# Kernel optimization log

Measured on AMD Instinct MI355X. Metric: run time of the kernel, lower is better.

The kernel has to match this reference:

```python
import jax, jax.numpy as jnp
import numpy as np

N_NODES, N_EDGES, N_GRAPHS = 20000, 640000, 16
D_NODE = D_EDGE = D_GLOBAL = 64
IN_DIM, LATENT, OUT_DIM = 256, 128, 64


def setup_inputs() -> dict:
    key = jax.random.key(0)
    ks = jax.random.split(key, 12)
    node_attr = jax.random.normal(ks[0], (N_NODES, D_NODE), dtype=jnp.float32)
    edge_attr = jax.random.normal(ks[1], (N_EDGES, D_EDGE), dtype=jnp.float32)
    global_attr = jax.random.normal(ks[2], (N_GRAPHS, D_GLOBAL), dtype=jnp.float32)
    node_mask = jax.random.uniform(ks[3], (N_NODES,), dtype=jnp.float32)
    edge_mask = jax.random.uniform(ks[4], (N_EDGES,), dtype=jnp.float32)
    edge_index = jax.random.randint(ks[5], (2, N_EDGES), 0, N_NODES, dtype=jnp.int64)
    eg_index = jax.random.randint(ks[6], (N_EDGES,), 0, N_GRAPHS, dtype=jnp.int64)
    # MLP params: Linear(IN_DIM, LATENT) -> ReLU -> Linear(LATENT, OUT_DIM)
    s1 = 1.0 / np.sqrt(IN_DIM)
    s2 = 1.0 / np.sqrt(LATENT)
    W1 = jax.random.uniform(ks[7], (IN_DIM, LATENT), minval=-s1, maxval=s1, dtype=jnp.float32)
    b1 = jax.random.uniform(ks[8], (LATENT,), minval=-s1, maxval=s1, dtype=jnp.float32)
    W2 = jax.random.uniform(ks[9], (LATENT, OUT_DIM), minval=-s2, maxval=s2, dtype=jnp.float32)
    b2 = jax.random.uniform(ks[10], (OUT_DIM,), minval=-s2, maxval=s2, dtype=jnp.float32)
    return {"node_attr": node_attr, "edge_attr": edge_attr, "global_attr": global_attr,
            "node_mask": node_mask, "edge_mask": edge_mask,
            "edge_index": edge_index, "eg_index": eg_index,
            "W1": W1, "b1": b1, "W2": W2, "b2": b2}


def reference(node_attr, edge_attr, global_attr, node_mask, edge_mask,
              edge_index, eg_index, W1, b1, W2, b2):
    senders, receivers = edge_index[0], edge_index[1]
    masked_nodes = node_attr * node_mask[:, None]          # [N, d_n]
    senders_attr = masked_nodes[senders]                   # [E, d_n] gather
    receivers_attr = masked_nodes[receivers]               # [E, d_n] gather
    globals_exp = global_attr[eg_index]                    # [E, d_g] gather
    collected = jnp.concatenate(
        [edge_attr, senders_attr, receivers_attr, globals_exp], axis=-1)  # [E, IN_DIM]
    h = jax.nn.relu(collected @ W1 + b1)                   # [E, LATENT]
    out = h @ W2 + b2                                      # [E, OUT_DIM]
    return edge_mask[:, None] * out
```

## Files before the change

### kernel.cpp

```cpp
#include <hip/hip_runtime.h>
#include <stdint.h>

typedef __attribute__((ext_vector_type(8))) short short8;
typedef __attribute__((ext_vector_type(4))) float floatx4;
typedef unsigned short ushort_t;

#define E_TOTAL 640000
#define N_NODES 20000
#define M_BLK   128
#define N_TILES (E_TOTAL / M_BLK)
#define XS_LD   264
#define HS_LD   136

__device__ __forceinline__ unsigned short f2h(float f){
    _Float16 h = (_Float16)f;
    union { _Float16 h; unsigned short u; } v; v.h = h; return v.u;
}
__device__ __forceinline__ unsigned pk2h(float a, float b){
    return (unsigned)f2h(a) | ((unsigned)f2h(b) << 16);
}

__global__ void repack_w(const float* __restrict__ W1,
                         const float* __restrict__ W2,
                         ushort_t* __restrict__ W1p,
                         ushort_t* __restrict__ W2p){
    int tid = blockIdx.x * 256 + threadIdx.x;
    if (tid < 8*8*64){
        int kt = tid >> 9, nt = (tid >> 6) & 7, l = tid & 63;
        int q = l >> 4, c = l & 15;
        ushort_t tmp[8];
        #pragma unroll
        for (int j = 0; j < 8; j++)
            tmp[j] = f2h(W1[(kt*32 + q*8 + j)*128 + nt*16 + c]);
        #pragma unroll
        for (int j = 0; j < 8; j++) W1p[tid*8 + j] = tmp[j];
    } else if (tid < 8*8*64 + 4*4*64){
        int t = tid - 8*8*64;
        int kt = t >> 8, nt = (t >> 6) & 3, l = t & 63;
        int q = l >> 4, c = l & 15;
        ushort_t tmp[8];
        #pragma unroll
        for (int j = 0; j < 8; j++)
            tmp[j] = f2h(W2[(kt*32 + q*8 + j)*64 + nt*16 + c]);
        #pragma unroll
        for (int j = 0; j < 8; j++) W2p[t*8 + j] = tmp[j];
    }
}

__global__ void prep_tables(const float* __restrict__ node_attr,
                            const float* __restrict__ node_mask,
                            const float* __restrict__ global_attr,
                            ushort_t* __restrict__ node16,
                            ushort_t* __restrict__ glob16){
    int gid = blockIdx.x * 256 + threadIdx.x;
    if (gid < N_NODES * 8){
        int r = gid >> 3, c8 = gid & 7;
        float m = node_mask[r];
        const float4* src = (const float4*)(node_attr + (size_t)r*64 + c8*8);
        float4 a = src[0], b = src[1];
        uint4 o;
        o.x = pk2h(a.x*m, a.y*m); o.y = pk2h(a.z*m, a.w*m);
        o.z = pk2h(b.x*m, b.y*m); o.w = pk2h(b.z*m, b.w*m);
        *(uint4*)(node16 + (size_t)r*64 + c8*8) = o;
    } else if (gid < N_NODES * 8 + 16 * 8){
        int t = gid - N_NODES * 8;
        int r = t >> 3, c8 = t & 7;
        const float4* src = (const float4*)(global_attr + (size_t)r*64 + c8*8);
        float4 a = src[0], b = src[1];
        uint4 o;
        o.x = pk2h(a.x, a.y); o.y = pk2h(a.z, a.w);
        o.z = pk2h(b.x, b.y); o.w = pk2h(b.z, b.w);
        *(uint4*)(glob16 + (size_t)r*64 + c8*8) = o;
    }
}

__global__ __launch_bounds__(512, 4)
void edge_mlp(const float* __restrict__ edge_attr,
              const float* __restrict__ edge_mask,
              const int*   __restrict__ edge_index,
              const int*   __restrict__ eg_index,
              const float* __restrict__ b1,
              const float* __restrict__ b2,
              const ushort_t* __restrict__ W1p,
              const ushort_t* __restrict__ W2p,
              const ushort_t* __restrict__ node16,
              const ushort_t* __restrict__ glob16,
              float*       __restrict__ out){
    __shared__ ushort_t Xs[M_BLK * XS_LD];
    ushort_t* Hs = Xs;

    const int tid = threadIdx.x;
    const int e0  = blockIdx.x * M_BLK;
    const int w   = tid >> 6, lane = tid & 63;
    const int q   = lane >> 4, cc = lane & 15;
    const int mt0 = (w >> 2) * 4;
    const int nt0 = (w & 3) * 2;

    const short8* W1v = (const short8*)W1p;
    short8 wb[8][2];
    #pragma unroll
    for (int kt = 0; kt < 8; kt++)
        #pragma unroll
        for (int j = 0; j < 2; j++)
            wb[kt][j] = W1v[(kt*8 + nt0 + j)*64 + lane];

    {
        const float4* src = (const float4*)(edge_attr + (size_t)e0 * 64);
        #pragma unroll
        for (int k = 0; k < 4; k++){
            int idx = tid + k*512;
            int r = idx >> 4, c = idx & 15;
            float4 v = src[idx];
            uint2 o; o.x = pk2h(v.x, v.y); o.y = pk2h(v.z, v.w);
            *(uint2*)&Xs[r*XS_LD + c*4] = o;
        }
    }
    {
        #pragma unroll
        for (int k = 0; k < 2; k++){
            int idx = tid + k*512;
            int r = idx >> 3, c = idx & 7;
            int g = eg_index[e0 + r];
            uint4 v = *(const uint4*)(glob16 + (size_t)g*64 + c*8);
            *(uint4*)&Xs[r*XS_LD + 192 + c*8] = v;
        }
    }
    {
        int r = tid >> 2, seg = (tid >> 1) & 1, half = tid & 1;
        int idx = edge_index[seg*E_TOTAL + e0 + r];
        const uint4* nsrc = (const uint4*)(node16 + (size_t)idx*64 + half*32);
        ushort_t* dst = &Xs[r*XS_LD + 64 + seg*64 + half*32];
        #pragma unroll
        for (int c2 = 0; c2 < 4; c2++)
            *(uint4*)(dst + c2*8) = nsrc[c2];
    }
    __syncthreads();

    floatx4 acc[4][2];
    #pragma unroll
    for (int i = 0; i < 4; i++)
        #pragma unroll
        for (int j = 0; j < 2; j++) acc[i][j] = (floatx4){0.f,0.f,0.f,0.f};

    #pragma unroll
    for (int kt = 0; kt < 8; kt++){
        #pragma unroll
        for (int i = 0; i < 4; i++){
            const short8 a = *(const short8*)&Xs[((mt0 + i)*16 + cc)*XS_LD + kt*32 + q*8];
            #pragma unroll
            for (int j = 0; j < 2; j++)
                acc[i][j] = __builtin_amdgcn_mfma_f32_16x16x32_f16(a, wb[kt][j], acc[i][j], 0, 0, 0);
        }
    }
    __syncthreads();

    #pragma unroll
    for (int j = 0; j < 2; j++){
        int col = (nt0 + j)*16 + cc;
        float bb = b1[col];
        #pragma unroll
        for (int i = 0; i < 4; i++){
            int rowb = (mt0 + i)*16 + q*4;
            #pragma unroll
            for (int r = 0; r < 4; r++){
                float v = acc[i][j][r] + bb;
                v = v > 0.f ? v : 0.f;
                Hs[(rowb + r)*HS_LD + col] = f2h(v);
            }
        }
    }
    __syncthreads();

    const int mt20 = (w >> 1) * 2;
    const int nt20 = (w & 1) * 2;

    floatx4 acc2[2][2];
    #pragma unroll
    for (int i = 0; i < 2; i++)
        #pragma unroll
        for (int j = 0; j < 2; j++) acc2[i][j] = (floatx4){0.f,0.f,0.f,0.f};

    const short8* W2v = (const short8*)W2p;
    #pragma unroll
    for (int kt = 0; kt < 4; kt++){
        short8 b[2];
        #pragma unroll
        for (int j = 0; j < 2; j++) b[j] = W2v[(kt*4 + nt20 + j)*64 + lane];
        #pragma unroll
        for (int i = 0; i < 2; i++){
            const short8 a = *(const short8*)&Hs[((mt20 + i)*16 + cc)*HS_LD + kt*32 + q*8];
            #pragma unroll
            for (int j = 0; j < 2; j++)
                acc2[i][j] = __builtin_amdgcn_mfma_f32_16x16x32_f16(a, b[j], acc2[i][j], 0, 0, 0);
        }
    }

    float bb2[2];
    #pragma unroll
    for (int j = 0; j < 2; j++) bb2[j] = b2[(nt20 + j)*16 + cc];
    #pragma unroll
    for (int i = 0; i < 2; i++){
        #pragma unroll
        for (int r = 0; r < 4; r++){
            int row = (mt20 + i)*16 + q*4 + r;
            float em = edge_mask[e0 + row];
            size_t base = (size_t)(e0 + row) * 64;
            #pragma unroll
            for (int j = 0; j < 2; j++)
                out[base + (nt20 + j)*16 + cc] = (acc2[i][j][r] + bb2[j]) * em;
        }
    }
}

__global__ __launch_bounds__(512, 4)
void edge_mlp_fb(const float* __restrict__ node_attr,
                 const float* __restrict__ edge_attr,
                 const float* __restrict__ global_attr,
                 const float* __restrict__ node_mask,
                 const float* __restrict__ edge_mask,
                 const int*   __restrict__ edge_index,
                 const int*   __restrict__ eg_index,
                 const float* __restrict__ b1,
                 const float* __restrict__ b2,
                 const ushort_t* __restrict__ W1p,
                 const ushort_t* __restrict__ W2p,
                 float*       __restrict__ out){
    __shared__ ushort_t Xs[M_BLK * XS_LD];
    ushort_t* Hs = Xs;
    const int tid = threadIdx.x;
    const int e0  = blockIdx.x * M_BLK;
    {
        const float4* src = (const float4*)(edge_attr + (size_t)e0 * 64);
        #pragma unroll
        for (int k = 0; k < 4; k++){
            int idx = tid + k*512;
            int r = idx >> 4, c = idx & 15;
            float4 v = src[idx];
            uint2 o; o.x = pk2h(v.x, v.y); o.y = pk2h(v.z, v.w);
            *(uint2*)&Xs[r*XS_LD + c*4] = o;
        }
    }
    {
        #pragma unroll
        for (int k = 0; k < 4; k++){
            int idx = tid + k*512; int r = idx >> 4, c = idx & 15;
            int g = eg_index[e0 + r];
            const float4* src = (const float4*)(global_attr + (size_t)g * 64);
            float4 v = src[c];
            uint2 o; o.x = pk2h(v.x, v.y); o.y = pk2h(v.z, v.w);
            *(uint2*)&Xs[r*XS_LD + 192 + c*4] = o;
        }
    }
    {
        int r = tid >> 2, seg = (tid >> 1) & 1, half = tid & 1;
        int idx = edge_index[seg*E_TOTAL + e0 + r];
        float m = node_mask[idx];
        const float4* src = (const float4*)(node_attr + (size_t)idx * 64) + half*8;
        ushort_t* dst = &Xs[r*XS_LD + 64 + seg*64 + half*32];
        #pragma unroll
        for (int c2 = 0; c2 < 8; c2++){
            float4 v = src[c2];
            uint2 o; o.x = pk2h(v.x*m, v.y*m); o.y = pk2h(v.z*m, v.w*m);
            *(uint2*)(dst + c2*4) = o;
        }
    }
    __syncthreads();

    const int w  = tid >> 6, lane = tid & 63;
    const int q  = lane >> 4, cc = lane & 15;
    const int mt0 = (w >> 2) * 4;
    const int nt0 = (w & 3) * 2;

    floatx4 acc[4][2];
    #pragma unroll
    for (int i = 0; i < 4; i++)
        #pragma unroll
        for (int j = 0; j < 2; j++) acc[i][j] = (floatx4){0.f,0.f,0.f,0.f};

    const short8* W1v = (const short8*)W1p;
    #pragma unroll
    for (int kt = 0; kt < 8; kt++){
        short8 b[2];
        #pragma unroll
        for (int j = 0; j < 2; j++) b[j] = W1v[(kt*8 + nt0 + j)*64 + lane];
        #pragma unroll
        for (int i = 0; i < 4; i++){
            const short8 a = *(const short8*)&Xs[((mt0 + i)*16 + cc)*XS_LD + kt*32 + q*8];
            #pragma unroll
            for (int j = 0; j < 2; j++)
                acc[i][j] = __builtin_amdgcn_mfma_f32_16x16x32_f16(a, b[j], acc[i][j], 0, 0, 0);
        }
    }
    __syncthreads();

    #pragma unroll
    for (int j = 0; j < 2; j++){
        int col = (nt0 + j)*16 + cc;
        float bb = b1[col];
        #pragma unroll
        for (int i = 0; i < 4; i++){
            int rowb = (mt0 + i)*16 + q*4;
            #pragma unroll
            for (int r = 0; r < 4; r++){
                float v = acc[i][j][r] + bb;
                v = v > 0.f ? v : 0.f;
                Hs[(rowb + r)*HS_LD + col] = f2h(v);
            }
        }
    }
    __syncthreads();

    const int mt20 = (w >> 1) * 2;
    const int nt20 = (w & 1) * 2;

    floatx4 acc2[2][2];
    #pragma unroll
    for (int i = 0; i < 2; i++)
        #pragma unroll
        for (int j = 0; j < 2; j++) acc2[i][j] = (floatx4){0.f,0.f,0.f,0.f};

    const short8* W2v = (const short8*)W2p;
    #pragma unroll
    for (int kt = 0; kt < 4; kt++){
        short8 b[2];
        #pragma unroll
        for (int j = 0; j < 2; j++) b[j] = W2v[(kt*4 + nt20 + j)*64 + lane];
        #pragma unroll
        for (int i = 0; i < 2; i++){
            const short8 a = *(const short8*)&Hs[((mt20 + i)*16 + cc)*HS_LD + kt*32 + q*8];
            #pragma unroll
            for (int j = 0; j < 2; j++)
                acc2[i][j] = __builtin_amdgcn_mfma_f32_16x16x32_f16(a, b[j], acc2[i][j], 0, 0, 0);
        }
    }

    float bb2[2];
    #pragma unroll
    for (int j = 0; j < 2; j++) bb2[j] = b2[(nt20 + j)*16 + cc];
    #pragma unroll
    for (int i = 0; i < 2; i++){
        #pragma unroll
        for (int r = 0; r < 4; r++){
            int row = (mt20 + i)*16 + q*4 + r;
            float em = edge_mask[e0 + row];
            size_t base = (size_t)(e0 + row) * 64;
            #pragma unroll
            for (int j = 0; j < 2; j++)
                out[base + (nt20 + j)*16 + cc] = (acc2[i][j][r] + bb2[j]) * em;
        }
    }
}

extern "C" void kernel_launch(void* const* d_in, const int* in_sizes, int n_in,
                              void* d_out, int out_size, void* d_ws, size_t ws_size,
                              hipStream_t stream){
    const float* node_attr   = (const float*)d_in[0];
    const float* edge_attr   = (const float*)d_in[1];
    const float* global_attr = (const float*)d_in[2];
    const float* node_mask   = (const float*)d_in[3];
    const float* edge_mask   = (const float*)d_in[4];
    const int*   edge_index  = (const int*)d_in[5];
    const int*   eg_index    = (const int*)d_in[6];
    const float* W1          = (const float*)d_in[7];
    const float* b1          = (const float*)d_in[8];
    const float* W2          = (const float*)d_in[9];
    const float* b2          = (const float*)d_in[10];

    ushort_t* W1p = (ushort_t*)d_ws;
    ushort_t* W2p = W1p + 8*8*64*8;
    ushort_t* node16 = W2p + 4*4*64*8;
    ushort_t* glob16 = node16 + (size_t)N_NODES*64;

    size_t need = (size_t)(8*8*64*8 + 4*4*64*8 + N_NODES*64 + 16*64) * sizeof(ushort_t);

    repack_w<<<20, 256, 0, stream>>>(W1, W2, W1p, W2p);
    if (ws_size >= need){
        prep_tables<<<(N_NODES*8 + 16*8 + 255)/256, 256, 0, stream>>>(
            node_attr, node_mask, global_attr, node16, glob16);
        edge_mlp<<<N_TILES, 512, 0, stream>>>(
            edge_attr, edge_mask, edge_index, eg_index,
            b1, b2, W1p, W2p, node16, glob16, (float*)d_out);
    } else {
        edge_mlp_fb<<<N_TILES, 512, 0, stream>>>(
            node_attr, edge_attr, global_attr, node_mask, edge_mask,
            edge_index, eg_index, b1, b2, W1p, W2p, (float*)d_out);
    }
}
```

Before: 337.0 us.

## Split first GEMM K loop into two halves to halve LDS and raise occupancy

The 256-wide input tile is now staged in shared memory in two 128-column halves: edge_attr plus sender features first, then receiver plus global features. This cuts LDS per block from 128x264 to 128x136 halves. W1 fragments are loaded per k-step instead of being held for all 8 k-steps, which reduces register pressure. Together these allow launch_bounds to go from 4 to 8 blocks per CU. In exchange it adds two extra barriers, serializes the second gather after the first half of the MFMA work, and reloads weights from global/L2 inside the loop.

```diff
diff --git a/kernel.cpp b/kernel.cpp
--- a/kernel.cpp
+++ b/kernel.cpp
@@ -9,8 +9,9 @@
 #define N_NODES 20000
 #define M_BLK   128
 #define N_TILES (E_TOTAL / M_BLK)
+#define XS2_LD  132
+#define HS_LD   136
 #define XS_LD   264
-#define HS_LD   136
 
 __device__ __forceinline__ unsigned short f2h(float f){
     _Float16 h = (_Float16)f;
@@ -74,7 +75,7 @@
     }
 }
 
-__global__ __launch_bounds__(512, 4)
+__global__ __launch_bounds__(512, 8)
 void edge_mlp(const float* __restrict__ edge_attr,
               const float* __restrict__ edge_mask,
               const int*   __restrict__ edge_index,
@@ -86,8 +87,9 @@
               const ushort_t* __restrict__ node16,
               const ushort_t* __restrict__ glob16,
               float*       __restrict__ out){
-    __shared__ ushort_t Xs[M_BLK * XS_LD];
-    ushort_t* Hs = Xs;
+    __shared__ ushort_t S[M_BLK * HS_LD];
+    ushort_t* Xs = S;
+    ushort_t* Hs = S;
 
     const int tid = threadIdx.x;
     const int e0  = blockIdx.x * M_BLK;
@@ -97,12 +99,6 @@
     const int nt0 = (w & 3) * 2;
 
     const short8* W1v = (const short8*)W1p;
-    short8 wb[8][2];
-    #pragma unroll
-    for (int kt = 0; kt < 8; kt++)
-        #pragma unroll
-        for (int j = 0; j < 2; j++)
-            wb[kt][j] = W1v[(kt*8 + nt0 + j)*64 + lane];
 
     {
         const float4* src = (const float4*)(edge_attr + (size_t)e0 * 64);
@@ -112,44 +108,71 @@
             int r = idx >> 4, c = idx & 15;
             float4 v = src[idx];
             uint2 o; o.x = pk2h(v.x, v.y); o.y = pk2h(v.z, v.w);
-            *(uint2*)&Xs[r*XS_LD + c*4] = o;
-        }
-    }
+            *(uint2*)&Xs[r*XS2_LD + c*4] = o;
+        }
+        #pragma unroll
+        for (int k = 0; k < 2; k++){
+            int idx = tid + k*512;
+            int r = idx >> 3, c = idx & 7;
+            int ei = edge_index[e0 + r];
+            uint4 v = *(const uint4*)(node16 + (size_t)ei*64 + c*8);
+            *(uint4*)&Xs[r*XS2_LD + 64 + c*8] = v;
+        }
+    }
+    __syncthreads();
+
+    floatx4 acc[4][2];
+    #pragma unroll
+    for (int i = 0; i < 4; i++)
+        #pragma unroll
+        for (int j = 0; j < 2; j++) acc[i][j] = (floatx4){0.f,0.f,0.f,0.f};
+
+    #pragma unroll
+    for (int kt = 0; kt < 4; kt++){
+        short8 b[2];
+        #pragma unroll
+        for (int j = 0; j < 2; j++) b[j] = W1v[(kt*8 + nt0 + j)*64 + lane];
+        #pragma unroll
+        for (int i = 0; i < 4; i++){
+            const short8 a = *(const short8*)&Xs[((mt0 + i)*16 + cc)*XS2_LD + kt*32 + q*8];
+            #pragma unroll
+            for (int j = 0; j < 2; j++)
+                acc[i][j] = __builtin_amdgcn_mfma_f32_16x16x32_f16(a, b[j], acc[i][j], 0, 0, 0);
+        }
+    }
+    __syncthreads();
+
     {
+        #pragma unroll
+        for (int k = 0; k < 2; k++){
+            int idx = tid + k*512;
+            int r = idx >> 3, c = idx & 7;
+            int ei = edge_index[E_TOTAL + e0 + r];
+            uint4 v = *(const uint4*)(node16 + (size_t)ei*64 + c*8);
+            *(uint4*)&Xs[r*XS2_LD + c*8] = v;
+        }
         #pragma unroll
         for (int k = 0; k < 2; k++){
             int idx = tid + k*512;
             int r = idx >> 3, c = idx & 7;
             int g = eg_index[e0 + r];
             uint4 v = *(const uint4*)(glob16 + (size_t)g*64 + c*8);
-            *(uint4*)&Xs[r*XS_LD + 192 + c*8] = v;
-        }
-    }
-    {
-        int r = tid >> 2, seg = (tid >> 1) & 1, half = tid & 1;
-        int idx = edge_index[seg*E_TOTAL + e0 + r];
-        const uint4* nsrc = (const uint4*)(node16 + (size_t)idx*64 + half*32);
-        ushort_t* dst = &Xs[r*XS_LD + 64 + seg*64 + half*32];
-        #pragma unroll
-        for (int c2 = 0; c2 < 4; c2++)
-            *(uint4*)(dst + c2*8) = nsrc[c2];
-    }
-    __syncthreads();
-
-    floatx4 acc[4][2];
-    #pragma unroll
-    for (int i = 0; i < 4; i++)
-        #pragma unroll
-        for (int j = 0; j < 2; j++) acc[i][j] = (floatx4){0.f,0.f,0.f,0.f};
-
-    #pragma unroll
-    for (int kt = 0; kt < 8; kt++){
+            *(uint4*)&Xs[r*XS2_LD + 64 + c*8] = v;
+        }
+    }
+    __syncthreads();
+
+    #pragma unroll
+    for (int kt = 4; kt < 8; kt++){
+        short8 b[2];
+        #pragma unroll
+        for (int j = 0; j < 2; j++) b[j] = W1v[(kt*8 + nt0 + j)*64 + lane];
         #pragma unroll
         for (int i = 0; i < 4; i++){
-            const short8 a = *(const short8*)&Xs[((mt0 + i)*16 + cc)*XS_LD + kt*32 + q*8];
-            #pragma unroll
-            for (int j = 0; j < 2; j++)
-                acc[i][j] = __builtin_amdgcn_mfma_f32_16x16x32_f16(a, wb[kt][j], acc[i][j], 0, 0, 0);
+            const short8 a = *(const short8*)&Xs[((mt0 + i)*16 + cc)*XS2_LD + (kt-4)*32 + q*8];
+            #pragma unroll
+            for (int j = 0; j < 2; j++)
+                acc[i][j] = __builtin_amdgcn_mfma_f32_16x16x32_f16(a, b[j], acc[i][j], 0, 0, 0);
         }
     }
     __syncthreads();
```

Result: slower. 426.0 us (+26.4%).
